# Kernel tuning notes

Measured on AMD Instinct MI355X. Metric: run time of the kernel, lower is better.

Reference implementation:

```python
import jax, jax.numpy as jnp
import numpy as np

D_MODEL = 2048
HEADS = 16
K = D_MODEL // HEADS  # 128
FFN = 8192


def rms_norm(x):
    # mean of squares over last dim, no eps (matches source)
    ms = jnp.mean(jnp.square(x), axis=2, keepdims=True)
    return x / jnp.sqrt(ms)


def setup_inputs() -> dict:
    key = jax.random.key(0)
    ks = jax.random.split(key, 9)
    s = D_MODEL ** (-0.5)
    B, S = 2, 2048
    return {
        "x_BSE": jax.random.normal(ks[0], (B, S, D_MODEL), jnp.float32),
        "w_q": jax.random.normal(ks[1], (D_MODEL, HEADS, K), jnp.float32) * s,
        "w_k": jax.random.normal(ks[2], (D_MODEL, HEADS, K), jnp.float32) * s,
        "w_v": jax.random.normal(ks[3], (D_MODEL, HEADS, K), jnp.float32) * s,
        "w_o": jax.random.normal(ks[4], (D_MODEL, HEADS, K), jnp.float32) * s,
        "w1": jax.random.normal(ks[5], (D_MODEL, FFN), jnp.float32) * s,
        "b1": jax.random.normal(ks[6], (1, FFN), jnp.float32) * s,
        "w2": jax.random.normal(ks[7], (FFN, D_MODEL), jnp.float32) * s,
        "b2": jax.random.normal(ks[8], (1, D_MODEL), jnp.float32) * s,
    }


def attention(x, w_q, w_k, w_v, w_o):
    q = jnp.einsum('bse,ehk->bshk', x, w_q)
    k = jnp.einsum('bme,ehk->bmhk', x, w_k)
    v = jnp.einsum('bme,ehk->bmhk', x, w_v)
    logits = jnp.einsum('bshk,bmhk->bshm', q, k) / jnp.sqrt(jnp.float32(K))
    S = x.shape[1]
    causal = jnp.arange(S)[:, None] >= jnp.arange(S)[None, :]  # [S, M]
    logits = jnp.where(causal[None, :, None, :], logits, -jnp.inf)
    probs = jax.nn.softmax(logits, axis=3)
    out = jnp.einsum('bshm,bmhk->bshk', probs, v)
    return jnp.einsum('bshk,ehk->bse', out, w_o)


def ffn(x, w1, b1, w2, b2):
    h = jnp.clip(x @ w1 + b1, 0.0, 6.0)  # ReLU6
    return h @ w2 + b2


def reference(x_BSE, w_q, w_k, w_v, w_o, w1, b1, w2, b2):
    x = x_BSE + attention(rms_norm(x_BSE), w_q, w_k, w_v, w_o)
    x = x + ffn(rms_norm(x), w1, b1, w2, b2)
    return x
```

## Files before the change

kernel.cpp:

```cpp
#include <hip/hip_runtime.h>
#include <hip/hip_bf16.h>
#include <stdint.h>

typedef __attribute__((ext_vector_type(8))) short bf16x8;
typedef __attribute__((ext_vector_type(4))) float f32x4;
typedef unsigned short ushort_t;

typedef __attribute__((address_space(1))) char as1_char;
typedef __attribute__((address_space(3))) char as3_char;

__device__ __forceinline__ void gload_lds16(const void* g, void* l) {
  __builtin_amdgcn_global_load_lds((as1_char*)g, (as3_char*)l, 16, 0, 0);
}

template <int N> __device__ __forceinline__ void waitvm() {
  asm volatile("s_waitcnt vmcnt(%0)" :: "n"(N) : "memory");
}

__device__ __forceinline__ unsigned short f2bf(float f) {
  union { float f; unsigned u; } c; c.f = f;
  unsigned u = c.u;
  return (unsigned short)((u + 0x7fffu + ((u >> 16) & 1u)) >> 16);
}

__global__ __launch_bounds__(256)
void rmsnorm_kernel(const float* __restrict__ x, unsigned short* __restrict__ out) {
  const int tok = blockIdx.x;
  const int tid = threadIdx.x;
  const float4* xr = (const float4*)(x + (size_t)tok * 2048);
  float4 a = xr[tid];
  float4 b = xr[tid + 256];
  float s = a.x*a.x + a.y*a.y + a.z*a.z + a.w*a.w
          + b.x*b.x + b.y*b.y + b.z*b.z + b.w*b.w;
  #pragma unroll
  for (int m = 1; m < 64; m <<= 1) s += __shfl_xor(s, m);
  __shared__ float ws4[4];
  if ((tid & 63) == 0) ws4[tid >> 6] = s;
  __syncthreads();
  const float tot = ws4[0] + ws4[1] + ws4[2] + ws4[3];
  const float r = rsqrtf(tot * (1.0f / 2048.0f));
  ushort4 o1, o2;
  o1.x = f2bf(a.x * r); o1.y = f2bf(a.y * r); o1.z = f2bf(a.z * r); o1.w = f2bf(a.w * r);
  o2.x = f2bf(b.x * r); o2.y = f2bf(b.y * r); o2.z = f2bf(b.z * r); o2.w = f2bf(b.w * r);
  ushort4* orow = (ushort4*)(out + (size_t)tok * 2048);
  orow[tid] = o1;
  orow[tid + 256] = o2;
}

__global__ __launch_bounds__(256)
void transpose_cvt(const float* __restrict__ in, unsigned short* __restrict__ out,
                   int R, int C) {
  __shared__ float t[32][33];
  const int c0 = blockIdx.x * 32, r0 = blockIdx.y * 32;
  const int tx = threadIdx.x, ty = threadIdx.y;
  #pragma unroll
  for (int i = 0; i < 4; i++)
    t[ty + 8 * i][tx] = in[(size_t)(r0 + ty + 8 * i) * C + (c0 + tx)];
  __syncthreads();
  #pragma unroll
  for (int i = 0; i < 4; i++)
    out[(size_t)(c0 + ty + 8 * i) * R + (r0 + tx)] = f2bf(t[tx][ty + 8 * i]);
}

__global__ __launch_bounds__(256)
void cvt_bf16_kernel(const float* __restrict__ in, unsigned short* __restrict__ out, int n4) {
  const int i = blockIdx.x * 256 + threadIdx.x;
  if (i < n4) {
    float4 v = ((const float4*)in)[i];
    ushort4 o; o.x = f2bf(v.x); o.y = f2bf(v.y); o.z = f2bf(v.z); o.w = f2bf(v.w);
    ((ushort4*)out)[i] = o;
  }
}

template <int EPI>
__global__ __launch_bounds__(512, 1)
void gemm_r3(const ushort_t* __restrict__ A, const ushort_t* __restrict__ B,
             int K, int N,
             ushort_t* ob0, ushort_t* ob1, ushort_t* ob2, float* outf,
             const float* __restrict__ res, const float* __restrict__ bias,
             int nbx) {
  constexpr int SLOT = 49152;
  __shared__ __align__(16) char smem[3 * SLOT];

  const int tid = threadIdx.x;
  const int lane = tid & 63;
  const int wid = tid >> 6;
  const int wm = wid >> 1, wn = wid & 1;
  const int ln15 = lane & 15, g = lane >> 4;

  int wg = blockIdx.x;
  const int cpx = gridDim.x >> 3;
  wg = (wg & 7) * cpx + (wg >> 3);
  const int bx = wg % nbx, by = wg / nbx;
  const int m0 = by * 256, n0 = bx * 128;

  const char* Ab = (const char*)(A + (size_t)m0 * K);
  const char* Bb = (const char*)(B + (size_t)n0 * K);
  const size_t rowb = (size_t)K * 2;
  const int NT = K >> 6;

  auto stage = [&](int t, int slot) {
    char* As = smem + slot * SLOT;
    char* Bs = As + 32768;
    const size_t kb = (size_t)t * 128;
    #pragma unroll
    for (int i = 0; i < 4; i++) {
      const int o = i * 8192 + tid * 16;
      const int row = o >> 7, col = o & 127;
      gload_lds16(Ab + (size_t)row * rowb + kb + (col ^ ((row & 7) << 4)), As + o);
    }
    #pragma unroll
    for (int i = 0; i < 2; i++) {
      const int o = i * 8192 + tid * 16;
      const int row = o >> 7, col = o & 127;
      gload_lds16(Bb + (size_t)row * rowb + kb + (col ^ ((row & 7) << 4)), Bs + o);
    }
  };

  f32x4 acc[4][4] = {};

  stage(0, 0);
  if (NT > 1) stage(1, 1);

  int slot = 0;
  for (int t = 0; t < NT; ++t) {
    if (t + 1 < NT) waitvm<6>(); else waitvm<0>();
    __builtin_amdgcn_s_barrier();

    const int slot2 = (slot + 2 >= 3) ? slot - 1 : slot + 2;
    if (t + 2 < NT) stage(t + 2, slot2);

    const char* As = smem + slot * SLOT;
    const char* Bs = As + 32768;

    bf16x8 af[4][2], bfm[4][2];
    #pragma unroll
    for (int mi = 0; mi < 4; mi++) {
      const int row = wm * 64 + mi * 16 + ln15;
      #pragma unroll
      for (int kk = 0; kk < 2; kk++)
        af[mi][kk] = *(const bf16x8*)(As + row * 128 + ((kk * 64 + g * 16) ^ ((row & 7) << 4)));
    }
    #pragma unroll
    for (int ni = 0; ni < 4; ni++) {
      const int row = wn * 64 + ni * 16 + ln15;
      #pragma unroll
      for (int kk = 0; kk < 2; kk++)
        bfm[ni][kk] = *(const bf16x8*)(Bs + row * 128 + ((kk * 64 + g * 16) ^ ((row & 7) << 4)));
    }

    __builtin_amdgcn_s_setprio(1);
    #pragma unroll
    for (int mi = 0; mi < 4; mi++)
      #pragma unroll
      for (int ni = 0; ni < 4; ni++)
        #pragma unroll
        for (int kk = 0; kk < 2; kk++)
          acc[mi][ni] = __builtin_amdgcn_mfma_f32_16x16x32_bf16(af[mi][kk], bfm[ni][kk], acc[mi][ni], 0, 0, 0);
    __builtin_amdgcn_s_setprio(0);

    slot = (slot + 1 >= 3) ? 0 : slot + 1;
  }

  #pragma unroll
  for (int mi = 0; mi < 4; mi++) {
    const int mrow = m0 + wm * 64 + mi * 16 + g * 4;
    #pragma unroll
    for (int ni = 0; ni < 4; ni++) {
      const int ncol = n0 + wn * 64 + ni * 16 + ln15;
      if (EPI == 0) {
        const int region = n0 >> 11;
        if (region == 0) {
          #pragma unroll
          for (int r = 0; r < 4; r++)
            ob0[(size_t)(mrow + r) * 2048 + ncol] = f2bf(acc[mi][ni][r]);
        } else if (region == 1) {
          #pragma unroll
          for (int r = 0; r < 4; r++)
            ob1[(size_t)(mrow + r) * 2048 + (ncol - 2048)] = f2bf(acc[mi][ni][r]);
        } else {
          const int bb = mrow >> 11, ss = mrow & 2047;
          const int ncv = ncol - 4096;
          const int hh = ncv >> 7, dd = ncv & 127;
          ushort4 v;
          v.x = f2bf(acc[mi][ni][0]); v.y = f2bf(acc[mi][ni][1]);
          v.z = f2bf(acc[mi][ni][2]); v.w = f2bf(acc[mi][ni][3]);
          *(ushort4*)(ob2 + ((size_t)((bb * 16 + hh) * 128 + dd)) * 2048 + ss) = v;
        }
      } else if (EPI == 2) {
        const float bv = bias[ncol];
        #pragma unroll
        for (int r = 0; r < 4; r++) {
          float v = acc[mi][ni][r] + bv;
          v = fminf(fmaxf(v, 0.0f), 6.0f);
          ob0[(size_t)(mrow + r) * N + ncol] = f2bf(v);
        }
      } else {
        const float bv = bias ? bias[ncol] : 0.0f;
        #pragma unroll
        for (int r = 0; r < 4; r++) {
          const size_t idx = (size_t)(mrow + r) * N + ncol;
          outf[idx] = res[idx] + acc[mi][ni][r] + bv;
        }
      }
    }
  }
}

__global__ __launch_bounds__(256)
void attn_kernel(const unsigned short* __restrict__ Qg,
                 const unsigned short* __restrict__ Kg,
                 const unsigned short* __restrict__ Vg,
                 unsigned short* __restrict__ Og) {
  __shared__ __align__(16) char smem[65536];
  const int tid = threadIdx.x, lane = tid & 63, wid = tid >> 6;
  const int g = lane >> 4, qq = lane & 15;
  const int pairx = blockIdx.x, h = blockIdx.y, b = blockIdx.z;

  auto stage = [&](int kv0, char* kdst, char* vdst) {
    #pragma unroll
    for (int i = 0; i < 4; i++) {
      const int oo = i * 4096 + tid * 16;
      const int rK = oo >> 8;
      const int sK = (oo & 255) ^ ((rK & 7) << 4);
      gload_lds16((const char*)Kg + ((size_t)(b * 2048 + kv0 + rK) * 2048 + h * 128) * 2 + sK,
                  kdst + oo);
      const int rV = oo >> 7;
      const int sV = (oo & 127) ^ ((rV & 7) << 4);
      gload_lds16((const char*)Vg + ((size_t)((b * 16 + h) * 128 + rV) * 2048 + kv0) * 2 + sV,
                  vdst + oo);
    }
  };

  for (int half = 0; half < 2; ++half) {
    const int qb = half ? (31 - pairx) : pairx;
    const int q0 = qb * 64;
    const int myq = q0 + wid * 16 + qq;
    const int nt = qb + 1;

    bf16x8 qf[4];
    const unsigned short* qp = Qg + ((size_t)(b * 2048 + myq)) * 2048 + h * 128 + g * 8;
    #pragma unroll
    for (int ks = 0; ks < 4; ks++) qf[ks] = *(const bf16x8*)(qp + ks * 32);

    stage(0, smem, smem + 16384);

    float m_run = -1e30f, l_run = 0.0f;
    f32x4 oacc[8] = {};

    for (int t = 0; t < nt; ++t) {
      const int cur = t & 1;
      char* kbc = cur ? smem + 32768 : smem;
      char* vbc = cur ? smem + 49152 : smem + 16384;
      char* kbn = cur ? smem : smem + 32768;
      char* vbn = cur ? smem + 16384 : smem + 49152;

      if (t + 1 < nt) {
        stage((t + 1) * 64, kbn, vbn);
        asm volatile("s_waitcnt vmcnt(8)" ::: "memory");
      } else {
        asm volatile("s_waitcnt vmcnt(0)" ::: "memory");
      }
      __builtin_amdgcn_s_barrier();
      asm volatile("" ::: "memory");

      const int kv0 = t * 64;

      f32x4 st[4] = {};
      __builtin_amdgcn_s_setprio(1);
      #pragma unroll
      for (int ks = 0; ks < 4; ks++) {
        #pragma unroll
        for (int f = 0; f < 4; f++) {
          const int row = f * 16 + qq;
          const int cb = ks * 64 + g * 16;
          bf16x8 kf = *(const bf16x8*)(kbc + row * 256 + (cb ^ ((row & 7) << 4)));
          st[f] = __builtin_amdgcn_mfma_f32_16x16x32_bf16(kf, qf[ks], st[f], 0, 0, 0);
        }
      }
      __builtin_amdgcn_s_setprio(0);

      float p[4][4];
      float tmax = -3.0e38f;
      const bool diag = (t == qb);
      #pragma unroll
      for (int f = 0; f < 4; f++) {
        #pragma unroll
        for (int r = 0; r < 4; r++) {
          float v = st[f][r] * 0.08838834764831845f;
          if (diag) {
            const int kv = kv0 + f * 16 + g * 4 + r;
            if (kv > myq) v = -3.0e38f;
          }
          p[f][r] = v;
          tmax = fmaxf(tmax, v);
        }
      }
      tmax = fmaxf(tmax, __shfl_xor(tmax, 16));
      tmax = fmaxf(tmax, __shfl_xor(tmax, 32));
      const float m_new = fmaxf(m_run, tmax);
      const float sf = __expf(m_run - m_new);
      m_run = m_new;
      float tsum = 0.0f;
      #pragma unroll
      for (int f = 0; f < 4; f++) {
        #pragma unroll
        for (int r = 0; r < 4; r++) {
          p[f][r] = __expf(p[f][r] - m_new);
          tsum += p[f][r];
        }
      }
      tsum += __shfl_xor(tsum, 16);
      tsum += __shfl_xor(tsum, 32);
      l_run = l_run * sf + tsum;

      unsigned pk[4][2];
      #pragma unroll
      for (int f = 0; f < 4; f++) {
        pk[f][0] = (unsigned)f2bf(p[f][0]) | ((unsigned)f2bf(p[f][1]) << 16);
        pk[f][1] = (unsigned)f2bf(p[f][2]) | ((unsigned)f2bf(p[f][3]) << 16);
      }
      bf16x8 pa[2];
      const int sel = g >> 1;
      #pragma unroll
      for (int ks2 = 0; ks2 < 2; ks2++) {
        unsigned d[4];
        #pragma unroll
        for (int u = 0; u < 2; u++) {
          const int sl = qq + (((2 * g + u) & 3) << 4);
          const unsigned lo0 = (unsigned)__shfl((int)pk[2 * ks2][0], sl);
          const unsigned hi0 = (unsigned)__shfl((int)pk[2 * ks2 + 1][0], sl);
          const unsigned lo1 = (unsigned)__shfl((int)pk[2 * ks2][1], sl);
          const unsigned hi1 = (unsigned)__shfl((int)pk[2 * ks2 + 1][1], sl);
          d[2 * u]     = sel ? hi0 : lo0;
          d[2 * u + 1] = sel ? hi1 : lo1;
        }
        union { unsigned u[4]; bf16x8 v; } cv;
        cv.u[0] = d[0]; cv.u[1] = d[1]; cv.u[2] = d[2]; cv.u[3] = d[3];
        pa[ks2] = cv.v;
      }

      float sfr[4];
      #pragma unroll
      for (int r = 0; r < 4; r++) sfr[r] = __shfl(sf, g * 4 + r);
      #pragma unroll
      for (int nf = 0; nf < 8; nf++) {
        oacc[nf][0] *= sfr[0]; oacc[nf][1] *= sfr[1];
        oacc[nf][2] *= sfr[2]; oacc[nf][3] *= sfr[3];
      }
      __builtin_amdgcn_s_setprio(1);
      #pragma unroll
      for (int nf = 0; nf < 8; nf++) {
        #pragma unroll
        for (int ks2 = 0; ks2 < 2; ks2++) {
          const int row = nf * 16 + qq;
          const int cb = ks2 * 64 + g * 16;
          bf16x8 vf = *(const bf16x8*)(vbc + row * 128 + (cb ^ ((row & 7) << 4)));
          oacc[nf] = __builtin_amdgcn_mfma_f32_16x16x32_bf16(pa[ks2], vf, oacc[nf], 0, 0, 0);
        }
      }
      __builtin_amdgcn_s_setprio(0);

      asm volatile("" ::: "memory");
      __builtin_amdgcn_s_barrier();
    }

    asm volatile("" ::: "memory");
    const float inv = 1.0f / l_run;
    float invr[4];
    #pragma unroll
    for (int r = 0; r < 4; r++) invr[r] = __shfl(inv, g * 4 + r);

    float* Osm = (float*)smem;
    #pragma unroll
    for (int nf = 0; nf < 8; nf++) {
      #pragma unroll
      for (int r = 0; r < 4; r++)
        Osm[(wid * 16 + g * 4 + r) * 132 + nf * 16 + qq] = oacc[nf][r] * invr[r];
    }
    __syncthreads();
    #pragma unroll
    for (int it = 0; it < 4; it++) {
      const int row = it * 16 + (tid >> 4);
      const int c0 = (tid & 15) * 8;
      const float* src = &Osm[row * 132 + c0];
      uint4 w;
      w.x = (unsigned)f2bf(src[0]) | ((unsigned)f2bf(src[1]) << 16);
      w.y = (unsigned)f2bf(src[2]) | ((unsigned)f2bf(src[3]) << 16);
      w.z = (unsigned)f2bf(src[4]) | ((unsigned)f2bf(src[5]) << 16);
      w.w = (unsigned)f2bf(src[6]) | ((unsigned)f2bf(src[7]) << 16);
      *(uint4*)(Og + (size_t)(b * 2048 + q0 + row) * 2048 + h * 128 + c0) = w;
    }
    __syncthreads();
  }
}

extern "C" void kernel_launch(void* const* d_in, const int* in_sizes, int n_in,
                              void* d_out, int out_size, void* d_ws, size_t ws_size,
                              hipStream_t stream) {
  (void)in_sizes; (void)n_in; (void)out_size; (void)ws_size;
  const float* x  = (const float*)d_in[0];
  const float* wq = (const float*)d_in[1];
  const float* wk = (const float*)d_in[2];
  const float* wv = (const float*)d_in[3];
  const float* wo = (const float*)d_in[4];
  const float* w1 = (const float*)d_in[5];
  const float* b1 = (const float*)d_in[6];
  const float* w2 = (const float*)d_in[7];
  const float* b2 = (const float*)d_in[8];
  float* out = (float*)d_out;
  char* ws = (char*)d_ws;

  ushort_t* wqkvT = (ushort_t*)(ws + 0);
  ushort_t* wqT = wqkvT;
  ushort_t* wkT = (ushort_t*)(ws + 8388608);
  ushort_t* wvT = (ushort_t*)(ws + 16777216);
  ushort_t* woC = (ushort_t*)(ws + 25165824);
  ushort_t* w1T = (ushort_t*)(ws + 33554432);
  ushort_t* w2T = (ushort_t*)(ws + 67108864);
  ushort_t* h1  = (ushort_t*)(ws + 100663296);
  ushort_t* Qb  = (ushort_t*)(ws + 117440512);
  ushort_t* Kb  = (ushort_t*)(ws + 134217728);
  ushort_t* Vt  = (ushort_t*)(ws + 150994944);
  ushort_t* hid = h1;
  ushort_t* att = (ushort_t*)(ws + 167772160);
  ushort_t* h2  = att;

  const dim3 tb(32, 8);
  transpose_cvt<<<dim3(64, 64), tb, 0, stream>>>(wq, wqT, 2048, 2048);
  transpose_cvt<<<dim3(64, 64), tb, 0, stream>>>(wk, wkT, 2048, 2048);
  transpose_cvt<<<dim3(64, 64), tb, 0, stream>>>(wv, wvT, 2048, 2048);
  cvt_bf16_kernel<<<4096, 256, 0, stream>>>(wo, woC, 1048576);
  transpose_cvt<<<dim3(256, 64), tb, 0, stream>>>(w1, w1T, 2048, 8192);
  transpose_cvt<<<dim3(64, 256), tb, 0, stream>>>(w2, w2T, 8192, 2048);

  rmsnorm_kernel<<<4096, 256, 0, stream>>>(x, h1);
  gemm_r3<0><<<48 * 16, 512, 0, stream>>>(h1, wqkvT, 2048, 6144,
                                          Qb, Kb, Vt, nullptr, nullptr, nullptr, 48);
  attn_kernel<<<dim3(16, 16, 2), 256, 0, stream>>>(Qb, Kb, Vt, att);
  gemm_r3<3><<<16 * 16, 512, 0, stream>>>(att, woC, 2048, 2048,
                                          nullptr, nullptr, nullptr, out, x, nullptr, 16);
  rmsnorm_kernel<<<4096, 256, 0, stream>>>(out, h2);
  gemm_r3<2><<<64 * 16, 512, 0, stream>>>(h2, w1T, 2048, 8192,
                                          hid, nullptr, nullptr, nullptr, nullptr, b1, 64);
  gemm_r3<3><<<16 * 16, 512, 0, stream>>>(hid, w2T, 8192, 2048,
                                          nullptr, nullptr, nullptr, out, out, b2, 16);
}
```

Before: 605.3 us.

## Add 256x256-tile 8-wave ping-pong GEMM for QKV and FFN1 projections

Introduces a new GEMM kernel with 256x256 output tiles, eight waves in a 2x4 layout, a double-buffered LDS with XOR swizzle, and a fine-grained interleaving of LDS fragment loads, global-to-LDS prefetches and MFMA quarters separated by barriers. It is used for the QKV projection and the first FFN GEMM, so each block reuses more data per loaded tile and global loads overlap with compute. The trade-off is fewer blocks (384 and 512) on the GPU's 256 CUs, which can leave some CUs idle in the last wave, plus higher register pressure from the 8x4 accumulator array.

```diff
diff --git a/kernel.cpp b/kernel.cpp
--- a/kernel.cpp
+++ b/kernel.cpp
@@ -74,6 +74,162 @@
 
 template <int EPI>
 __global__ __launch_bounds__(512, 1)
+void gemm8p(const ushort_t* __restrict__ A, const ushort_t* __restrict__ B,
+            int K, int N,
+            ushort_t* ob0, ushort_t* ob1, ushort_t* ob2,
+            const float* __restrict__ bias, int nbx) {
+  __shared__ __align__(16) char smem[131072];
+  const int tid = threadIdx.x;
+  const int lane = tid & 63;
+  const int wid = tid >> 6;
+  const int wm = wid >> 2, wn = wid & 3;
+  const int ln15 = lane & 15, g = lane >> 4;
+
+  int wg = blockIdx.x;
+  const int cpx = gridDim.x >> 3;
+  wg = (wg & 7) * cpx + (wg >> 3);
+  const int bx = wg % nbx, by = wg / nbx;
+  const int m0 = by * 256, n0 = bx * 256;
+
+  const char* Ab = (const char*)(A + (size_t)m0 * K);
+  const char* Bb = (const char*)(B + (size_t)n0 * K);
+  const size_t rowb = (size_t)K * 2;
+  const int ITERS = K >> 7;
+
+  auto stA = [&](int t, int h) {
+    char* dst = smem + ((t & 1) << 16) + (h << 14);
+    const size_t kb = (size_t)t << 7;
+    #pragma unroll
+    for (int j = 0; j < 2; j++) {
+      const int o = j * 8192 + tid * 16;
+      const int lr = o >> 7, col = o & 127;
+      const int grow = (lr & 63) + (h << 6) + ((lr >> 6) << 7);
+      gload_lds16(Ab + (size_t)grow * rowb + kb + (col ^ ((lr & 7) << 4)), dst + o);
+    }
+  };
+  auto stB = [&](int t, int h) {
+    char* dst = smem + ((t & 1) << 16) + 32768 + (h << 14);
+    const size_t kb = (size_t)t << 7;
+    #pragma unroll
+    for (int j = 0; j < 2; j++) {
+      const int o = j * 8192 + tid * 16;
+      const int lr = o >> 7, col = o & 127;
+      const int grow = (lr & 31) + (h << 5) + ((lr >> 5) << 6);
+      gload_lds16(Bb + (size_t)grow * rowb + kb + (col ^ ((lr & 7) << 4)), dst + o);
+    }
+  };
+
+  f32x4 acc[8][4] = {};
+  bf16x8 af[8], bfr[4];
+  const int lra = wm * 64 + ln15;
+  const int lrb = wn * 32 + ln15;
+
+  auto ldA = [&](int c, int mh) {
+    const char* base = smem + (c << 16) + (mh << 14);
+    #pragma unroll
+    for (int mi = 0; mi < 4; mi++) {
+      const int lr = lra + mi * 16;
+      #pragma unroll
+      for (int kk = 0; kk < 2; kk++)
+        af[mi * 2 + kk] = *(const bf16x8*)(base + lr * 128 + ((kk * 64 + g * 16) ^ ((lr & 7) << 4)));
+    }
+  };
+  auto ldB = [&](int c, int nh) {
+    const char* base = smem + (c << 16) + 32768 + (nh << 14);
+    #pragma unroll
+    for (int ni = 0; ni < 2; ni++) {
+      const int lr = lrb + ni * 16;
+      #pragma unroll
+      for (int kk = 0; kk < 2; kk++)
+        bfr[ni * 2 + kk] = *(const bf16x8*)(base + lr * 128 + ((kk * 64 + g * 16) ^ ((lr & 7) << 4)));
+    }
+  };
+
+#define MFQ(MH, NH)                                                              \
+  __builtin_amdgcn_s_barrier();                                                  \
+  asm volatile("s_waitcnt lgkmcnt(0)" ::: "memory");                             \
+  __builtin_amdgcn_sched_barrier(0);                                             \
+  __builtin_amdgcn_s_setprio(1);                                                 \
+  _Pragma("unroll")                                                              \
+  for (int mi = 0; mi < 4; mi++)                                                 \
+    _Pragma("unroll")                                                            \
+    for (int ni = 0; ni < 2; ni++)                                               \
+      _Pragma("unroll")                                                          \
+      for (int kk = 0; kk < 2; kk++)                                             \
+        acc[(MH) * 4 + mi][(NH) * 2 + ni] = __builtin_amdgcn_mfma_f32_16x16x32_bf16( \
+            af[mi * 2 + kk], bfr[ni * 2 + kk], acc[(MH) * 4 + mi][(NH) * 2 + ni], 0, 0, 0); \
+  __builtin_amdgcn_s_setprio(0);                                                 \
+  __builtin_amdgcn_s_barrier();
+
+  stA(0, 0); stB(0, 0); stB(0, 1); stA(0, 1);
+  stA(1, 0); stB(1, 1); stA(1, 1);
+  waitvm<6>();
+  __builtin_amdgcn_s_barrier();
+
+  for (int i = 0; i < ITERS; ++i) {
+    const int a = 2 * i, b = a + 1;
+    const bool pf = (i + 1 < ITERS);
+    ldA(0, 0); ldB(0, 0); stB(b, 0);
+    MFQ(0, 0)
+    ldB(0, 1); if (pf) stA(a + 2, 0);
+    MFQ(0, 1)
+    ldA(0, 1); if (pf) stB(a + 2, 1);
+    MFQ(1, 1)
+    ldB(0, 0); if (pf) stA(a + 2, 1);
+    if (pf) waitvm<6>(); else waitvm<0>();
+    MFQ(1, 0)
+    ldA(1, 0); ldB(1, 0); if (pf) stB(a + 2, 0);
+    MFQ(0, 0)
+    ldB(1, 1); if (pf) stA(b + 2, 0);
+    MFQ(0, 1)
+    ldA(1, 1); if (pf) stB(b + 2, 1);
+    MFQ(1, 1)
+    ldB(1, 0); if (pf) stA(b + 2, 1);
+    if (pf) waitvm<6>();
+    MFQ(1, 0)
+  }
+#undef MFQ
+
+  #pragma unroll
+  for (int mig = 0; mig < 8; mig++) {
+    const int mrow = m0 + wm * 128 + (mig >> 2) * 64 + (mig & 3) * 16 + g * 4;
+    #pragma unroll
+    for (int nig = 0; nig < 4; nig++) {
+      const int ncol = n0 + wn * 64 + (nig >> 1) * 32 + (nig & 1) * 16 + ln15;
+      if (EPI == 0) {
+        const int region = n0 >> 11;
+        if (region == 0) {
+          #pragma unroll
+          for (int r = 0; r < 4; r++)
+            ob0[(size_t)(mrow + r) * 2048 + ncol] = f2bf(acc[mig][nig][r]);
+        } else if (region == 1) {
+          #pragma unroll
+          for (int r = 0; r < 4; r++)
+            ob1[(size_t)(mrow + r) * 2048 + (ncol - 2048)] = f2bf(acc[mig][nig][r]);
+        } else {
+          const int bb = mrow >> 11, ss = mrow & 2047;
+          const int ncv = ncol - 4096;
+          const int hh = ncv >> 7, dd = ncv & 127;
+          ushort4 v;
+          v.x = f2bf(acc[mig][nig][0]); v.y = f2bf(acc[mig][nig][1]);
+          v.z = f2bf(acc[mig][nig][2]); v.w = f2bf(acc[mig][nig][3]);
+          *(ushort4*)(ob2 + ((size_t)((bb * 16 + hh) * 128 + dd)) * 2048 + ss) = v;
+        }
+      } else {
+        const float bv = bias[ncol];
+        #pragma unroll
+        for (int r = 0; r < 4; r++) {
+          float v = acc[mig][nig][r] + bv;
+          v = fminf(fmaxf(v, 0.0f), 6.0f);
+          ob0[(size_t)(mrow + r) * N + ncol] = f2bf(v);
+        }
+      }
+    }
+  }
+}
+
+template <int EPI>
+__global__ __launch_bounds__(512, 1)
 void gemm_r3(const ushort_t* __restrict__ A, const ushort_t* __restrict__ B,
              int K, int N,
              ushort_t* ob0, ushort_t* ob1, ushort_t* ob2, float* outf,
@@ -168,26 +324,7 @@
     #pragma unroll
     for (int ni = 0; ni < 4; ni++) {
       const int ncol = n0 + wn * 64 + ni * 16 + ln15;
-      if (EPI == 0) {
-        const int region = n0 >> 11;
-        if (region == 0) {
-          #pragma unroll
-          for (int r = 0; r < 4; r++)
-            ob0[(size_t)(mrow + r) * 2048 + ncol] = f2bf(acc[mi][ni][r]);
-        } else if (region == 1) {
-          #pragma unroll
-          for (int r = 0; r < 4; r++)
-            ob1[(size_t)(mrow + r) * 2048 + (ncol - 2048)] = f2bf(acc[mi][ni][r]);
-        } else {
-          const int bb = mrow >> 11, ss = mrow & 2047;
-          const int ncv = ncol - 4096;
-          const int hh = ncv >> 7, dd = ncv & 127;
-          ushort4 v;
-          v.x = f2bf(acc[mi][ni][0]); v.y = f2bf(acc[mi][ni][1]);
-          v.z = f2bf(acc[mi][ni][2]); v.w = f2bf(acc[mi][ni][3]);
-          *(ushort4*)(ob2 + ((size_t)((bb * 16 + hh) * 128 + dd)) * 2048 + ss) = v;
-        }
-      } else if (EPI == 2) {
+      if (EPI == 2) {
         const float bv = bias[ncol];
         #pragma unroll
         for (int r = 0; r < 4; r++) {
@@ -435,14 +572,14 @@
   transpose_cvt<<<dim3(64, 256), tb, 0, stream>>>(w2, w2T, 8192, 2048);
 
   rmsnorm_kernel<<<4096, 256, 0, stream>>>(x, h1);
-  gemm_r3<0><<<48 * 16, 512, 0, stream>>>(h1, wqkvT, 2048, 6144,
-                                          Qb, Kb, Vt, nullptr, nullptr, nullptr, 48);
+  gemm8p<0><<<24 * 16, 512, 0, stream>>>(h1, wqkvT, 2048, 6144,
+                                         Qb, Kb, Vt, nullptr, 24);
   attn_kernel<<<dim3(16, 16, 2), 256, 0, stream>>>(Qb, Kb, Vt, att);
   gemm_r3<3><<<16 * 16, 512, 0, stream>>>(att, woC, 2048, 2048,
                                           nullptr, nullptr, nullptr, out, x, nullptr, 16);
   rmsnorm_kernel<<<4096, 256, 0, stream>>>(out, h2);
-  gemm_r3<2><<<64 * 16, 512, 0, stream>>>(h2, w1T, 2048, 8192,
-                                          hid, nullptr, nullptr, nullptr, nullptr, b1, 64);
+  gemm8p<2><<<32 * 16, 512, 0, stream>>>(h2, w1T, 2048, 8192,
+                                         hid, nullptr, nullptr, b1, 32);
   gemm_r3<3><<<16 * 16, 512, 0, stream>>>(hid, w2T, 8192, 2048,
                                           nullptr, nullptr, nullptr, out, out, b2, 16);
 }
```

Result: no change. 604.7 us (-0.1%).

## Double-buffer GEMM register fragments and widen attention blocks to 128 queries

Applied to the files above, without the earlier changes.

The GEMM main loop is unrolled by two and ping-pongs between two register fragment sets, so LDS reads for the next tile overlap MFMAs on the current one. Launch bounds are raised to ask for two workgroups per CU. The attention kernel moves to 512 threads handling 128-query blocks, with K/V staging split across more threads and a two-pass output writeback. The aim is better latency hiding and K/V reuse, at the cost of higher register pressure. The 147KB LDS footprint likely still caps GEMM occupancy at one workgroup.

```diff
diff --git a/kernel.cpp b/kernel.cpp
--- a/kernel.cpp
+++ b/kernel.cpp
@@ -73,7 +73,7 @@
 }
 
 template <int EPI>
-__global__ __launch_bounds__(512, 1)
+__global__ __launch_bounds__(512, 2)
 void gemm_r3(const ushort_t* __restrict__ A, const ushort_t* __restrict__ B,
              int K, int N,
              ushort_t* ob0, ushort_t* ob1, ushort_t* ob2, float* outf,
@@ -99,8 +99,8 @@
   const size_t rowb = (size_t)K * 2;
   const int NT = K >> 6;
 
-  auto stage = [&](int t, int slot) {
-    char* As = smem + slot * SLOT;
+  auto stage = [&](int t, int s) {
+    char* As = smem + s * SLOT;
     char* Bs = As + 32768;
     const size_t kb = (size_t)t * 128;
     #pragma unroll
@@ -118,22 +118,11 @@
   };
 
   f32x4 acc[4][4] = {};
-
-  stage(0, 0);
-  if (NT > 1) stage(1, 1);
-
-  int slot = 0;
-  for (int t = 0; t < NT; ++t) {
-    if (t + 1 < NT) waitvm<6>(); else waitvm<0>();
-    __builtin_amdgcn_s_barrier();
-
-    const int slot2 = (slot + 2 >= 3) ? slot - 1 : slot + 2;
-    if (t + 2 < NT) stage(t + 2, slot2);
-
-    const char* As = smem + slot * SLOT;
+  bf16x8 afA[4][2], bfA[4][2], afB[4][2], bfB[4][2];
+
+  auto LD = [&](int s, bf16x8 (&af)[4][2], bf16x8 (&bf)[4][2]) {
+    const char* As = smem + s * SLOT;
     const char* Bs = As + 32768;
-
-    bf16x8 af[4][2], bfm[4][2];
     #pragma unroll
     for (int mi = 0; mi < 4; mi++) {
       const int row = wm * 64 + mi * 16 + ln15;
@@ -146,20 +135,56 @@
       const int row = wn * 64 + ni * 16 + ln15;
       #pragma unroll
       for (int kk = 0; kk < 2; kk++)
-        bfm[ni][kk] = *(const bf16x8*)(Bs + row * 128 + ((kk * 64 + g * 16) ^ ((row & 7) << 4)));
-    }
-
+        bf[ni][kk] = *(const bf16x8*)(Bs + row * 128 + ((kk * 64 + g * 16) ^ ((row & 7) << 4)));
+    }
+  };
+  auto MM = [&](bf16x8 (&af)[4][2], bf16x8 (&bf)[4][2]) {
     __builtin_amdgcn_s_setprio(1);
     #pragma unroll
-    for (int mi = 0; mi < 4; mi++)
-      #pragma unroll
-      for (int ni = 0; ni < 4; ni++)
-        #pragma unroll
-        for (int kk = 0; kk < 2; kk++)
-          acc[mi][ni] = __builtin_amdgcn_mfma_f32_16x16x32_bf16(af[mi][kk], bfm[ni][kk], acc[mi][ni], 0, 0, 0);
+    for (int kk = 0; kk < 2; kk++)
+      #pragma unroll
+      for (int mi = 0; mi < 4; mi++)
+        #pragma unroll
+        for (int ni = 0; ni < 4; ni++)
+          acc[mi][ni] = __builtin_amdgcn_mfma_f32_16x16x32_bf16(af[mi][kk], bf[ni][kk], acc[mi][ni], 0, 0, 0);
     __builtin_amdgcn_s_setprio(0);
-
-    slot = (slot + 1 >= 3) ? 0 : slot + 1;
+  };
+
+  stage(0, 0); stage(1, 1);
+  waitvm<6>();
+  __builtin_amdgcn_s_barrier();
+  LD(0, afA, bfA);
+
+  int slot = 0;
+  for (int t = 0; t < NT; t += 2) {
+    {
+      const int s2 = (slot + 2 >= 3) ? slot - 1 : slot + 2;
+      if (t + 2 < NT) stage(t + 2, s2);
+      if (t + 2 < NT) waitvm<6>(); else waitvm<0>();
+      asm volatile("s_waitcnt lgkmcnt(0)" ::: "memory");
+      __builtin_amdgcn_s_barrier();
+      const int s1 = (slot + 1 >= 3) ? 0 : slot + 1;
+      LD(s1, afB, bfB);
+      __builtin_amdgcn_sched_barrier(0x7);
+      MM(afA, bfA);
+    }
+    {
+      const int sB = (slot + 1 >= 3) ? 0 : slot + 1;
+      const int s3 = (sB + 2 >= 3) ? sB - 1 : sB + 2;
+      if (t + 3 < NT) stage(t + 3, s3);
+      if (t + 3 < NT) waitvm<6>(); else waitvm<0>();
+      asm volatile("s_waitcnt lgkmcnt(0)" ::: "memory");
+      __builtin_amdgcn_s_barrier();
+      if (t + 2 < NT) {
+        const int s1 = (sB + 1 >= 3) ? 0 : sB + 1;
+        LD(s1, afA, bfA);
+        __builtin_amdgcn_sched_barrier(0x7);
+        MM(afB, bfB);
+      } else {
+        MM(afB, bfB);
+      }
+    }
+    slot = (slot + 2 >= 3) ? slot - 1 : slot + 2;
   }
 
   #pragma unroll
@@ -207,7 +232,7 @@
   }
 }
 
-__global__ __launch_bounds__(256)
+__global__ __launch_bounds__(512, 2)
 void attn_kernel(const unsigned short* __restrict__ Qg,
                  const unsigned short* __restrict__ Kg,
                  const unsigned short* __restrict__ Vg,
@@ -219,8 +244,8 @@
 
   auto stage = [&](int kv0, char* kdst, char* vdst) {
     #pragma unroll
-    for (int i = 0; i < 4; i++) {
-      const int oo = i * 4096 + tid * 16;
+    for (int i = 0; i < 2; i++) {
+      const int oo = i * 8192 + tid * 16;
       const int rK = oo >> 8;
       const int sK = (oo & 255) ^ ((rK & 7) << 4);
       gload_lds16((const char*)Kg + ((size_t)(b * 2048 + kv0 + rK) * 2048 + h * 128) * 2 + sK,
@@ -233,10 +258,10 @@
   };
 
   for (int half = 0; half < 2; ++half) {
-    const int qb = half ? (31 - pairx) : pairx;
-    const int q0 = qb * 64;
+    const int qb8 = half ? (15 - pairx) : pairx;
+    const int q0 = qb8 * 128;
     const int myq = q0 + wid * 16 + qq;
-    const int nt = qb + 1;
+    const int nt = 2 * qb8 + 2;
 
     bf16x8 qf[4];
     const unsigned short* qp = Qg + ((size_t)(b * 2048 + myq)) * 2048 + h * 128 + g * 8;
@@ -257,7 +282,7 @@
 
       if (t + 1 < nt) {
         stage((t + 1) * 64, kbn, vbn);
-        asm volatile("s_waitcnt vmcnt(8)" ::: "memory");
+        asm volatile("s_waitcnt vmcnt(4)" ::: "memory");
       } else {
         asm volatile("s_waitcnt vmcnt(0)" ::: "memory");
       }
@@ -282,7 +307,7 @@
 
       float p[4][4];
       float tmax = -3.0e38f;
-      const bool diag = (t == qb);
+      const bool diag = (kv0 + 63 > q0 + wid * 16);
       #pragma unroll
       for (int f = 0; f < 4; f++) {
         #pragma unroll
@@ -350,9 +375,9 @@
       }
       __builtin_amdgcn_s_setprio(1);
       #pragma unroll
-      for (int nf = 0; nf < 8; nf++) {
-        #pragma unroll
-        for (int ks2 = 0; ks2 < 2; ks2++) {
+      for (int ks2 = 0; ks2 < 2; ks2++) {
+        #pragma unroll
+        for (int nf = 0; nf < 8; nf++) {
           const int row = nf * 16 + qq;
           const int cb = ks2 * 64 + g * 16;
           bf16x8 vf = *(const bf16x8*)(vbc + row * 128 + (cb ^ ((row & 7) << 4)));
@@ -373,25 +398,31 @@
 
     float* Osm = (float*)smem;
     #pragma unroll
-    for (int nf = 0; nf < 8; nf++) {
-      #pragma unroll
-      for (int r = 0; r < 4; r++)
-        Osm[(wid * 16 + g * 4 + r) * 132 + nf * 16 + qq] = oacc[nf][r] * invr[r];
-    }
-    __syncthreads();
-    #pragma unroll
-    for (int it = 0; it < 4; it++) {
-      const int row = it * 16 + (tid >> 4);
-      const int c0 = (tid & 15) * 8;
-      const float* src = &Osm[row * 132 + c0];
-      uint4 w;
-      w.x = (unsigned)f2bf(src[0]) | ((unsigned)f2bf(src[1]) << 16);
-      w.y = (unsigned)f2bf(src[2]) | ((unsigned)f2bf(src[3]) << 16);
-      w.z = (unsigned)f2bf(src[4]) | ((unsigned)f2bf(src[5]) << 16);
-      w.w = (unsigned)f2bf(src[6]) | ((unsigned)f2bf(src[7]) << 16);
-      *(uint4*)(Og + (size_t)(b * 2048 + q0 + row) * 2048 + h * 128 + c0) = w;
-    }
-    __syncthreads();
+    for (int pass = 0; pass < 2; ++pass) {
+      if ((wid >> 2) == pass) {
+        const int w4 = wid & 3;
+        #pragma unroll
+        for (int nf = 0; nf < 8; nf++) {
+          #pragma unroll
+          for (int r = 0; r < 4; r++)
+            Osm[(w4 * 16 + g * 4 + r) * 132 + nf * 16 + qq] = oacc[nf][r] * invr[r];
+        }
+      }
+      __syncthreads();
+      #pragma unroll
+      for (int it = 0; it < 2; it++) {
+        const int row = it * 32 + (tid >> 4);
+        const int c0 = (tid & 15) * 8;
+        const float* src = &Osm[row * 132 + c0];
+        uint4 w;
+        w.x = (unsigned)f2bf(src[0]) | ((unsigned)f2bf(src[1]) << 16);
+        w.y = (unsigned)f2bf(src[2]) | ((unsigned)f2bf(src[3]) << 16);
+        w.z = (unsigned)f2bf(src[4]) | ((unsigned)f2bf(src[5]) << 16);
+        w.w = (unsigned)f2bf(src[6]) | ((unsigned)f2bf(src[7]) << 16);
+        *(uint4*)(Og + (size_t)(b * 2048 + q0 + pass * 64 + row) * 2048 + h * 128 + c0) = w;
+      }
+      __syncthreads();
+    }
   }
 }
 
@@ -437,7 +468,7 @@
   rmsnorm_kernel<<<4096, 256, 0, stream>>>(x, h1);
   gemm_r3<0><<<48 * 16, 512, 0, stream>>>(h1, wqkvT, 2048, 6144,
                                           Qb, Kb, Vt, nullptr, nullptr, nullptr, 48);
-  attn_kernel<<<dim3(16, 16, 2), 256, 0, stream>>>(Qb, Kb, Vt, att);
+  attn_kernel<<<dim3(8, 16, 2), 512, 0, stream>>>(Qb, Kb, Vt, att);
   gemm_r3<3><<<16 * 16, 512, 0, stream>>>(att, woC, 2048, 2048,
                                           nullptr, nullptr, nullptr, out, x, nullptr, 16);
   rmsnorm_kernel<<<4096, 256, 0, stream>>>(out, h2);
```

Result: slower. 1.448 ms (+139.2%).
